# Optimization experiments

Measured on AMD Instinct MI355X. Metric: run time of the kernel, lower is better.

Reference implementation:

```python
import jax, jax.numpy as jnp
import numpy as np

CANVAS_W = 1024.0
CANVAS_H = 1024.0
EPS = 1e-8
GOLDEN = 1.618
ALIGN_THRESH = 5.0


def _mse(p, t):
    return jnp.mean((p - t) ** 2)


def _smooth_l1(p, t):
    d = jnp.abs(p - t)
    return jnp.mean(jnp.where(d < 1.0, 0.5 * d * d, d - 0.5))


def setup_inputs() -> dict:
    key = jax.random.key(0)
    k1, k2, k3, k4 = jax.random.split(key, 4)
    B, N, D = 64, 256, 6
    return {
        "predicted_noise": jax.random.normal(k1, (B, N, D), dtype=jnp.float32),
        "target_noise": jax.random.normal(k2, (B, N, D), dtype=jnp.float32),
        "predicted_layout": jax.random.normal(k3, (B, N, D), dtype=jnp.float32),
        "target_layout": jax.random.normal(k4, (B, N, D), dtype=jnp.float32),
        "element_mask": jnp.ones((B, N), dtype=jnp.float32),
    }


def _iou_loss(pred, target):
    # boxes are (x, y, w, h)
    px1, py1 = pred[..., 0], pred[..., 1]
    px2, py2 = px1 + pred[..., 2], py1 + pred[..., 3]
    tx1, ty1 = target[..., 0], target[..., 1]
    tx2, ty2 = tx1 + target[..., 2], ty1 + target[..., 3]
    inter = jnp.maximum(jnp.minimum(px2, tx2) - jnp.maximum(px1, tx1), 0.0) * \
            jnp.maximum(jnp.minimum(py2, ty2) - jnp.maximum(py1, ty1), 0.0)
    pa = pred[..., 2] * pred[..., 3]
    ta = target[..., 2] * target[..., 3]
    iou = inter / (pa + ta - inter + EPS)
    return jnp.mean(1.0 - iou)


def _loss(predicted_noise, target_noise, predicted_layout, target_layout, element_mask):
    B, N, _ = predicted_noise.shape
    mask3 = element_mask[..., None]  # [B,N,1]
    pn = predicted_noise * mask3
    tn = target_noise * mask3
    pl = predicted_layout * mask3
    tl = target_layout * mask3

    npairs = N * (N - 1) / 2.0
    tri = jnp.triu(jnp.ones((N, N), dtype=pl.dtype), k=1)  # i<j pair mask
    pair_valid = element_mask[:, :, None] * element_mask[:, None, :]  # [B,N,N]

    # ---- noise loss (SmoothL1) ----
    noise_loss = _smooth_l1(pn, tn)

    # ---- position loss: MSE + 0.5*IoU ----
    position_loss = _mse(pl[..., :4], tl[..., :4]) + 0.5 * _iou_loss(pl[..., :4], tl[..., :4])

    # ---- layer loss: MSE + 0.3*pairwise ranking BCE ----
    p_layer, t_layer = pl[..., 4], tl[..., 4]
    diff = p_layer[:, None, :] - p_layer[:, :, None]          # [b,i,j] = p_j - p_i
    y = (t_layer[:, :, None] < t_layer[:, None, :]).astype(pl.dtype)
    # BCE(sigmoid(diff), y): -log sigmoid(d)=softplus(-d); torch clamps log terms at 100
    bce = y * jnp.minimum(jax.nn.softplus(-diff), 100.0) + \
          (1.0 - y) * jnp.minimum(jax.nn.softplus(diff), 100.0)
    ranking = jnp.sum(bce * tri) / (B * npairs)
    layer_loss = _mse(p_layer, t_layer) + 0.3 * ranking

    # ---- confidence loss ----
    confidence_loss = _mse(pl[..., 5], tl[..., 5])

    # ---- aesthetic loss ----
    aspect = pl[..., 2] / (pl[..., 3] + EPS)
    golden = jnp.mean(jnp.abs(aspect - GOLDEN))
    areas = pl[..., 2] * pl[..., 3] * element_mask
    size_harm = jnp.mean(jnp.std(areas, axis=1, ddof=1)) / (jnp.mean(areas) + EPS)
    cx = (pl[..., 0] + pl[..., 2] / 2) * element_mask
    cy = (pl[..., 1] + pl[..., 3] / 2) * element_mask
    valid_count = jnp.sum(element_mask, axis=1, keepdims=True)  # [B,1]
    # NOTE: faithful to original broadcasting ([B] / [B,1] -> [B,B])
    ocx = jnp.sum(cx, axis=1) / (valid_count + EPS)
    ocy = jnp.sum(cy, axis=1) / (valid_count + EPS)
    balance = jnp.mean(jnp.abs(ocx - CANVAS_W / 2) / (CANVAS_W / 2) +
                       jnp.abs(ocy - CANVAS_H / 2) / (CANVAS_H / 2))
    aesthetic_loss = 0.1 * golden + 0.2 * size_harm + 0.15 * balance

    # ---- overlap loss (pairwise) ----
    x1, y1, w, h = pl[..., 0], pl[..., 1], pl[..., 2], pl[..., 3]
    x2, y2 = x1 + w, y1 + h
    iw = jnp.maximum(jnp.minimum(x2[:, :, None], x2[:, None, :]) -
                     jnp.maximum(x1[:, :, None], x1[:, None, :]), 0.0)
    ih = jnp.maximum(jnp.minimum(y2[:, :, None], y2[:, None, :]) -
                     jnp.maximum(y1[:, :, None], y1[:, None, :]), 0.0)
    area = w * h
    min_area = jnp.minimum(area[:, :, None], area[:, None, :])
    overlap_ratio = (iw * ih) / (min_area + EPS) * pair_valid
    overlap_loss = jnp.sum(overlap_ratio * tri) / (B * npairs)

    # ---- alignment loss (6 edge types, pairwise) ----
    edges = jnp.stack([x1, x2, y1, y2, x1 + w / 2, y1 + h / 2], axis=0)  # [6,B,N]
    dist = jnp.abs(edges[:, :, :, None] - edges[:, :, None, :])          # [6,B,N,N]
    pen = jnp.where(dist < ALIGN_THRESH, dist / ALIGN_THRESH, 0.0) * pair_valid[None]
    alignment_loss = jnp.sum(pen * tri) / (B * 6.0 * npairs)

    total = (noise_loss + 1.0 * position_loss + 0.5 * layer_loss +
             0.3 * confidence_loss + 0.2 * aesthetic_loss +
             0.8 * overlap_loss + 0.4 * alignment_loss)
    return total


def reference(predicted_noise, target_noise, predicted_layout, target_layout, element_mask):
    return _loss(predicted_noise, target_noise, predicted_layout, target_layout, element_mask)
```

## Files before the change

kernel.cpp:

```cpp
#include <hip/hip_runtime.h>
#include <math.h>

#define NB 64
#define NN 256
#define NPAIRS 32640.0f
#define EPSF 1e-8f

#define PB(q) ((q) * 64)
#define PW(q) (704 + (q) * 512)

__device__ __forceinline__ float block_sum(float v, float* sred) {
    const int tid = threadIdx.x;
    #pragma unroll
    for (int off = 32; off > 0; off >>= 1) v += __shfl_down(v, off, 64);
    __syncthreads();
    if ((tid & 63) == 0) sred[tid >> 6] = v;
    __syncthreads();
    return sred[0] + sred[1] + sred[2] + sred[3];
}

__device__ __forceinline__ void block_sum3(float a, float b, float c, float* sred,
                                           float& ra, float& rb, float& rc) {
    const int tid = threadIdx.x;
    #pragma unroll
    for (int off = 32; off > 0; off >>= 1) {
        a += __shfl_down(a, off, 64);
        b += __shfl_down(b, off, 64);
        c += __shfl_down(c, off, 64);
    }
    __syncthreads();
    if ((tid & 63) == 0) {
        const int w = tid >> 6;
        sred[w] = a; sred[4 + w] = b; sred[8 + w] = c;
    }
    __syncthreads();
    ra = sred[0] + sred[1] + sred[2]  + sred[3];
    rb = sred[4] + sred[5] + sred[6]  + sred[7];
    rc = sred[8] + sred[9] + sred[10] + sred[11];
}

__global__ __launch_bounds__(256) void loss_main(
    const float* __restrict__ pn, const float* __restrict__ tn,
    const float* __restrict__ pl, const float* __restrict__ tl,
    const float* __restrict__ mask, float* __restrict__ ws)
{
    __shared__ float4 sA[NN], sB[NN];
    __shared__ float2 sC[NN];
    __shared__ float sred[12];

    const int b     = blockIdx.x >> 3;
    const int chunk = blockIdx.x & 7;
    const int i     = threadIdx.x;
    const int e     = b * NN + i;
    const float m   = mask[e];

    const float2* pl2 = (const float2*)pl;
    const float2* tl2 = (const float2*)tl;
    const int r2 = e * 3;
    const float2 pla = pl2[r2 + 0], plb = pl2[r2 + 1], plc = pl2[r2 + 2];
    const float2 tlc = tl2[r2 + 2];

    const float p0 = pla.x * m, p1 = pla.y * m,
                p2 = plb.x * m, p3 = plb.y * m,
                p4 = plc.x * m, p5 = plc.y * m;
    const float t4 = tlc.x * m, t5 = tlc.y * m;

    const float x2v = p0 + p2, y2v = p1 + p3;
    const float areav = p2 * p3;
    const float cxe = p0 + 0.5f * p2, cye = p1 + 0.5f * p3;

    sA[i] = make_float4(p0, p1, x2v, y2v);
    sB[i] = make_float4(cxe, cye, areav, p4);
    sC[i] = make_float2(t4, m);
    __syncthreads();

    float rank = 0.f, ovl = 0.f, aln = 0.f;
    const int dd0 = chunk * 16 + 1;
    #pragma unroll 8
    for (int dd = dd0; dd < dd0 + 16; ++dd) {
        int j = (i + dd) & 255;
        if (dd == 128 && i >= 128) continue;
        float4 aj = sA[j];
        float4 bj = sB[j];
        float2 cj = sC[j];
        float pv = m * cj.y;
        float ow = fmaxf(fminf(x2v, aj.z) - fmaxf(p0, aj.x), 0.f);
        float oh = fmaxf(fminf(y2v, aj.w) - fmaxf(p1, aj.y), 0.f);
        ovl += ow * oh / (fminf(areav, bj.z) + EPSF) * pv;
        float pen = 0.f, d;
        d = fabsf(p0  - aj.x); pen += (d < 5.f) ? d : 0.f;
        d = fabsf(x2v - aj.z); pen += (d < 5.f) ? d : 0.f;
        d = fabsf(p1  - aj.y); pen += (d < 5.f) ? d : 0.f;
        d = fabsf(y2v - aj.w); pen += (d < 5.f) ? d : 0.f;
        d = fabsf(cxe - bj.x); pen += (d < 5.f) ? d : 0.f;
        d = fabsf(cye - bj.y); pen += (d < 5.f) ? d : 0.f;
        aln += pen * 0.2f * pv;
        bool ilt = (i < j);
        float dlo = ilt ? (bj.w - p4) : (p4 - bj.w);
        float ylo = (ilt ? (t4 < cj.x) : (cj.x < t4)) ? 1.f : 0.f;
        float sp  = __logf(1.f + __expf(-fabsf(dlo)));
        float sp_pos = sp + fmaxf(dlo, 0.f);
        float sp_neg = sp + fmaxf(-dlo, 0.f);
        rank += ylo * fminf(sp_neg, 100.f) + (1.f - ylo) * fminf(sp_pos, 100.f);
    }

    {
        float sr, so, sa;
        block_sum3(rank, ovl, aln, sred, sr, so, sa);
        if (i == 0) {
            ws[PW(0) + blockIdx.x] = sr;
            ws[PW(1) + blockIdx.x] = so;
            ws[PW(2) + blockIdx.x] = sa;
        }
    }

    float s;
    switch (chunk) {
    case 0: {
        const float2* pn2 = (const float2*)pn;
        const float2* tn2 = (const float2*)tn;
        float noise = 0.f;
        #pragma unroll
        for (int k = 0; k < 3; ++k) {
            float2 a = pn2[r2 + k], bb = tn2[r2 + k];
            float d0 = fabsf(a.x * m - bb.x * m);
            float d1 = fabsf(a.y * m - bb.y * m);
            noise += (d0 < 1.f) ? 0.5f * d0 * d0 : d0 - 0.5f;
            noise += (d1 < 1.f) ? 0.5f * d1 * d1 : d1 - 0.5f;
        }
        s = block_sum(noise, sred); if (i == 0) ws[PB(0) + b] = s;
        break; }
    case 1: {
        const float2 tla = tl2[r2 + 0], tlb = tl2[r2 + 1];
        const float t0 = tla.x * m, t1 = tla.y * m,
                    t2 = tlb.x * m, t3 = tlb.y * m;
        float posmse = (p0 - t0) * (p0 - t0) + (p1 - t1) * (p1 - t1)
                     + (p2 - t2) * (p2 - t2) + (p3 - t3) * (p3 - t3);
        const float tx2 = t0 + t2, ty2 = t1 + t3;
        float iw = fmaxf(fminf(x2v, tx2) - fmaxf(p0, t0), 0.f);
        float ih = fmaxf(fminf(y2v, ty2) - fmaxf(p1, t1), 0.f);
        float inter = iw * ih;
        float iouL = 1.f - inter / (areav + t2 * t3 - inter + EPSF);
        float s0, s1, s2;
        block_sum3(posmse, iouL, 0.f, sred, s0, s1, s2);
        if (i == 0) { ws[PB(1) + b] = s0; ws[PB(2) + b] = s1; }
        break; }
    case 2: {
        float lmse = (p4 - t4) * (p4 - t4);
        float cmse = (p5 - t5) * (p5 - t5);
        float s0, s1, s2;
        block_sum3(lmse, cmse, 0.f, sred, s0, s1, s2);
        if (i == 0) { ws[PB(3) + b] = s0; ws[PB(4) + b] = s1; }
        break; }
    case 3: {
        float golden = fabsf(p2 / (p3 + EPSF) - 1.618f);
        s = block_sum(golden, sred); if (i == 0) ws[PB(5) + b] = s;
        break; }
    case 4: {
        float areaA = areav * m;
        s = block_sum(areaA, sred); if (i == 0) ws[PB(6) + b] = s;
        break; }
    case 5: {
        float areaA = areav * m;
        s = block_sum(areaA * areaA, sred); if (i == 0) ws[PB(7) + b] = s;
        break; }
    case 6: {
        float cxA = cxe * m, cyA = cye * m;
        float s0, s1, s2;
        block_sum3(cxA, cyA, 0.f, sred, s0, s1, s2);
        if (i == 0) { ws[PB(8) + b] = s0; ws[PB(9) + b] = s1; }
        break; }
    default: {
        s = block_sum(m, sred); if (i == 0) ws[PB(10) + b] = s;
        break; }
    }
}

__global__ __launch_bounds__(256) void loss_final(
    const float* __restrict__ ws, float* __restrict__ out)
{
    __shared__ float sred[12];
    __shared__ float bcx[NB], bcy[NB], bvc[NB];
    const int t = threadIdx.x;

    float v_noise = 0.f, v_pos = 0.f, v_iou = 0.f, v_lm = 0.f, v_cf = 0.f,
          v_go = 0.f, v_ar = 0.f, v_std = 0.f;
    if (t < NB) {
        v_noise = ws[PB(0) + t];
        v_pos   = ws[PB(1) + t];
        v_iou   = ws[PB(2) + t];
        v_lm    = ws[PB(3) + t];
        v_cf    = ws[PB(4) + t];
        v_go    = ws[PB(5) + t];
        v_ar    = ws[PB(6) + t];
        float a2 = ws[PB(7) + t];
        float var = (a2 - v_ar * v_ar * (1.f / 256.f)) * (1.f / 255.f);
        v_std = sqrtf(fmaxf(var, 0.f));
        bcx[t] = ws[PB(8) + t];
        bcy[t] = ws[PB(9) + t];
        bvc[t] = ws[PB(10) + t];
    }
    float v_rank = ws[PW(0) + t] + ws[PW(0) + 256 + t];
    float v_ovl  = ws[PW(1) + t] + ws[PW(1) + 256 + t];
    float v_aln  = ws[PW(2) + t] + ws[PW(2) + 256 + t];
    __syncthreads();

    float v_bal = 0.f;
    if (t < NB) {
        float inv = 1.f / (bvc[t] + EPSF);
        for (int j = 0; j < NB; ++j) {
            v_bal += fabsf(bcx[j] * inv - 512.f) * (1.f / 512.f)
                   + fabsf(bcy[j] * inv - 512.f) * (1.f / 512.f);
        }
    }

    float S_noise, S_pos, S_iou, S_lm, S_cf, S_go, S_ar, S_std, S_bal,
          S_rank, S_ovl, S_aln;
    block_sum3(v_noise, v_pos, v_iou, sred, S_noise, S_pos, S_iou);
    block_sum3(v_lm,    v_cf,  v_go,  sred, S_lm,    S_cf,  S_go);
    block_sum3(v_ar,    v_std, v_bal, sred, S_ar,    S_std, S_bal);
    block_sum3(v_rank,  v_ovl, v_aln, sred, S_rank,  S_ovl, S_aln);

    if (t == 0) {
        const float BN = 64.f * 256.f;
        float noise_loss = S_noise / (BN * 6.f);
        float position   = S_pos / (BN * 4.f) + 0.5f * (S_iou / BN);
        float layer      = S_lm / BN + 0.3f * (S_rank / (64.f * NPAIRS));
        float conf       = S_cf / BN;
        float golden     = S_go / BN;
        float size_harm  = (S_std / 64.f) / (S_ar / BN + EPSF);
        float balance    = S_bal / 4096.f;
        float aes        = 0.1f * golden + 0.2f * size_harm + 0.15f * balance;
        float ovl        = S_ovl / (64.f * NPAIRS);
        float aln        = S_aln / (64.f * 6.f * NPAIRS);
        out[0] = noise_loss + position + 0.5f * layer + 0.3f * conf
               + 0.2f * aes + 0.8f * ovl + 0.4f * aln;
    }
}

extern "C" void kernel_launch(void* const* d_in, const int* in_sizes, int n_in,
                              void* d_out, int out_size, void* d_ws, size_t ws_size,
                              hipStream_t stream) {
    const float* pn   = (const float*)d_in[0];
    const float* tn   = (const float*)d_in[1];
    const float* pl   = (const float*)d_in[2];
    const float* tl   = (const float*)d_in[3];
    const float* mask = (const float*)d_in[4];
    float* ws  = (float*)d_ws;
    float* out = (float*)d_out;
    hipLaunchKernelGGL(loss_main, dim3(512), dim3(256), 0, stream,
                       pn, tn, pl, tl, mask, ws);
    hipLaunchKernelGGL(loss_final, dim3(1), dim3(256), 0, stream, ws, out);
}
```

Measured before the change: 71.79 us.

## Split pairwise work into 16 chunks per batch and simplify final reduction

Doubles the grid to 1024 blocks so each block handles 8 pair offsets instead of 16, and spreads the per-element side terms across 11 chunks with one block reduction each. The final kernel shrinks to a single 64-thread wavefront that uses shuffles instead of shared memory and block barriers. This targets latency from too few blocks relative to the CU count and from serial reductions. In exchange, every block reloads and stages the whole batch into shared memory, so redundant loads double, and the final kernel now sums 16 partials per slot.

After: 71.37 us. Within noise of the previous version (-0.6%).

```diff
diff --git a/kernel.cpp b/kernel.cpp
--- a/kernel.cpp
+++ b/kernel.cpp
@@ -7,7 +7,7 @@
 #define EPSF 1e-8f
 
 #define PB(q) ((q) * 64)
-#define PW(q) (704 + (q) * 512)
+#define PW(q) (704 + (q) * 1024)
 
 __device__ __forceinline__ float block_sum(float v, float* sred) {
     const int tid = threadIdx.x;
@@ -37,6 +37,12 @@
     ra = sred[0] + sred[1] + sred[2]  + sred[3];
     rb = sred[4] + sred[5] + sred[6]  + sred[7];
     rc = sred[8] + sred[9] + sred[10] + sred[11];
+}
+
+__device__ __forceinline__ float wave_sum(float v) {
+    #pragma unroll
+    for (int off = 32; off > 0; off >>= 1) v += __shfl_down(v, off, 64);
+    return v;
 }
 
 __global__ __launch_bounds__(256) void loss_main(
@@ -48,8 +54,8 @@
     __shared__ float2 sC[NN];
     __shared__ float sred[12];
 
-    const int b     = blockIdx.x >> 3;
-    const int chunk = blockIdx.x & 7;
+    const int b     = blockIdx.x >> 4;
+    const int chunk = blockIdx.x & 15;
     const int i     = threadIdx.x;
     const int e     = b * NN + i;
     const float m   = mask[e];
@@ -75,9 +81,10 @@
     __syncthreads();
 
     float rank = 0.f, ovl = 0.f, aln = 0.f;
-    const int dd0 = chunk * 16 + 1;
-    #pragma unroll 8
-    for (int dd = dd0; dd < dd0 + 16; ++dd) {
+    const int dd0 = chunk * 8 + 1;
+    #pragma unroll
+    for (int k = 0; k < 8; ++k) {
+        const int dd = dd0 + k;
         int j = (i + dd) & 255;
         if (dd == 128 && i >= 128) continue;
         float4 aj = sA[j];
@@ -114,7 +121,8 @@
         }
     }
 
-    float s;
+    float v = 0.f;
+    bool have = true;
     switch (chunk) {
     case 0: {
         const float2* pn2 = (const float2*)pn;
@@ -128,98 +136,89 @@
             noise += (d0 < 1.f) ? 0.5f * d0 * d0 : d0 - 0.5f;
             noise += (d1 < 1.f) ? 0.5f * d1 * d1 : d1 - 0.5f;
         }
-        s = block_sum(noise, sred); if (i == 0) ws[PB(0) + b] = s;
+        v = noise;
         break; }
     case 1: {
         const float2 tla = tl2[r2 + 0], tlb = tl2[r2 + 1];
         const float t0 = tla.x * m, t1 = tla.y * m,
                     t2 = tlb.x * m, t3 = tlb.y * m;
-        float posmse = (p0 - t0) * (p0 - t0) + (p1 - t1) * (p1 - t1)
-                     + (p2 - t2) * (p2 - t2) + (p3 - t3) * (p3 - t3);
+        v = (p0 - t0) * (p0 - t0) + (p1 - t1) * (p1 - t1)
+          + (p2 - t2) * (p2 - t2) + (p3 - t3) * (p3 - t3);
+        break; }
+    case 2: {
+        const float2 tla = tl2[r2 + 0], tlb = tl2[r2 + 1];
+        const float t0 = tla.x * m, t1 = tla.y * m,
+                    t2 = tlb.x * m, t3 = tlb.y * m;
         const float tx2 = t0 + t2, ty2 = t1 + t3;
         float iw = fmaxf(fminf(x2v, tx2) - fmaxf(p0, t0), 0.f);
         float ih = fmaxf(fminf(y2v, ty2) - fmaxf(p1, t1), 0.f);
         float inter = iw * ih;
-        float iouL = 1.f - inter / (areav + t2 * t3 - inter + EPSF);
-        float s0, s1, s2;
-        block_sum3(posmse, iouL, 0.f, sred, s0, s1, s2);
-        if (i == 0) { ws[PB(1) + b] = s0; ws[PB(2) + b] = s1; }
+        v = 1.f - inter / (areav + t2 * t3 - inter + EPSF);
         break; }
-    case 2: {
-        float lmse = (p4 - t4) * (p4 - t4);
-        float cmse = (p5 - t5) * (p5 - t5);
-        float s0, s1, s2;
-        block_sum3(lmse, cmse, 0.f, sred, s0, s1, s2);
-        if (i == 0) { ws[PB(3) + b] = s0; ws[PB(4) + b] = s1; }
-        break; }
-    case 3: {
-        float golden = fabsf(p2 / (p3 + EPSF) - 1.618f);
-        s = block_sum(golden, sred); if (i == 0) ws[PB(5) + b] = s;
-        break; }
-    case 4: {
-        float areaA = areav * m;
-        s = block_sum(areaA, sred); if (i == 0) ws[PB(6) + b] = s;
-        break; }
-    case 5: {
-        float areaA = areav * m;
-        s = block_sum(areaA * areaA, sred); if (i == 0) ws[PB(7) + b] = s;
-        break; }
-    case 6: {
-        float cxA = cxe * m, cyA = cye * m;
-        float s0, s1, s2;
-        block_sum3(cxA, cyA, 0.f, sred, s0, s1, s2);
-        if (i == 0) { ws[PB(8) + b] = s0; ws[PB(9) + b] = s1; }
-        break; }
-    default: {
-        s = block_sum(m, sred); if (i == 0) ws[PB(10) + b] = s;
-        break; }
-    }
-}
-
-__global__ __launch_bounds__(256) void loss_final(
+    case 3: v = (p4 - t4) * (p4 - t4); break;
+    case 4: v = (p5 - t5) * (p5 - t5); break;
+    case 5: v = fabsf(p2 / (p3 + EPSF) - 1.618f); break;
+    case 6: v = areav * m; break;
+    case 7: { float a = areav * m; v = a * a; break; }
+    case 8: v = cxe * m; break;
+    case 9: v = cye * m; break;
+    case 10: v = m; break;
+    default: have = false; break;
+    }
+    if (have) {
+        float s = block_sum(v, sred);
+        if (i == 0) ws[PB(chunk) + b] = s;
+    }
+}
+
+__global__ __launch_bounds__(64) void loss_final(
     const float* __restrict__ ws, float* __restrict__ out)
 {
-    __shared__ float sred[12];
-    __shared__ float bcx[NB], bcy[NB], bvc[NB];
     const int t = threadIdx.x;
 
-    float v_noise = 0.f, v_pos = 0.f, v_iou = 0.f, v_lm = 0.f, v_cf = 0.f,
-          v_go = 0.f, v_ar = 0.f, v_std = 0.f;
-    if (t < NB) {
-        v_noise = ws[PB(0) + t];
-        v_pos   = ws[PB(1) + t];
-        v_iou   = ws[PB(2) + t];
-        v_lm    = ws[PB(3) + t];
-        v_cf    = ws[PB(4) + t];
-        v_go    = ws[PB(5) + t];
-        v_ar    = ws[PB(6) + t];
-        float a2 = ws[PB(7) + t];
-        float var = (a2 - v_ar * v_ar * (1.f / 256.f)) * (1.f / 255.f);
-        v_std = sqrtf(fmaxf(var, 0.f));
-        bcx[t] = ws[PB(8) + t];
-        bcy[t] = ws[PB(9) + t];
-        bvc[t] = ws[PB(10) + t];
-    }
-    float v_rank = ws[PW(0) + t] + ws[PW(0) + 256 + t];
-    float v_ovl  = ws[PW(1) + t] + ws[PW(1) + 256 + t];
-    float v_aln  = ws[PW(2) + t] + ws[PW(2) + 256 + t];
-    __syncthreads();
-
+    float v_noise = ws[PB(0) + t];
+    float v_pos   = ws[PB(1) + t];
+    float v_iou   = ws[PB(2) + t];
+    float v_lm    = ws[PB(3) + t];
+    float v_cf    = ws[PB(4) + t];
+    float v_go    = ws[PB(5) + t];
+    float v_ar    = ws[PB(6) + t];
+    float a2      = ws[PB(7) + t];
+    float v_cx    = ws[PB(8) + t];
+    float v_cy    = ws[PB(9) + t];
+    float v_vc    = ws[PB(10) + t];
+    float var   = (a2 - v_ar * v_ar * (1.f / 256.f)) * (1.f / 255.f);
+    float v_std = sqrtf(fmaxf(var, 0.f));
+
+    float v_rank = 0.f, v_ovl = 0.f, v_aln = 0.f;
+    #pragma unroll
+    for (int k = 0; k < 16; ++k) {
+        v_rank += ws[PW(0) + k * 64 + t];
+        v_ovl  += ws[PW(1) + k * 64 + t];
+        v_aln  += ws[PW(2) + k * 64 + t];
+    }
+
+    float inv = 1.f / (v_vc + EPSF);
     float v_bal = 0.f;
-    if (t < NB) {
-        float inv = 1.f / (bvc[t] + EPSF);
-        for (int j = 0; j < NB; ++j) {
-            v_bal += fabsf(bcx[j] * inv - 512.f) * (1.f / 512.f)
-                   + fabsf(bcy[j] * inv - 512.f) * (1.f / 512.f);
-        }
-    }
-
-    float S_noise, S_pos, S_iou, S_lm, S_cf, S_go, S_ar, S_std, S_bal,
-          S_rank, S_ovl, S_aln;
-    block_sum3(v_noise, v_pos, v_iou, sred, S_noise, S_pos, S_iou);
-    block_sum3(v_lm,    v_cf,  v_go,  sred, S_lm,    S_cf,  S_go);
-    block_sum3(v_ar,    v_std, v_bal, sred, S_ar,    S_std, S_bal);
-    block_sum3(v_rank,  v_ovl, v_aln, sred, S_rank,  S_ovl, S_aln);
+    for (int j = 0; j < NB; ++j) {
+        float cxj = __shfl(v_cx, j, 64);
+        float cyj = __shfl(v_cy, j, 64);
+        v_bal += fabsf(cxj * inv - 512.f) * (1.f / 512.f)
+               + fabsf(cyj * inv - 512.f) * (1.f / 512.f);
+    }
+
+    float S_noise = wave_sum(v_noise);
+    float S_pos   = wave_sum(v_pos);
+    float S_iou   = wave_sum(v_iou);
+    float S_lm    = wave_sum(v_lm);
+    float S_cf    = wave_sum(v_cf);
+    float S_go    = wave_sum(v_go);
+    float S_ar    = wave_sum(v_ar);
+    float S_std   = wave_sum(v_std);
+    float S_bal   = wave_sum(v_bal);
+    float S_rank  = wave_sum(v_rank);
+    float S_ovl   = wave_sum(v_ovl);
+    float S_aln   = wave_sum(v_aln);
 
     if (t == 0) {
         const float BN = 64.f * 256.f;
@@ -248,7 +247,7 @@
     const float* mask = (const float*)d_in[4];
     float* ws  = (float*)d_ws;
     float* out = (float*)d_out;
-    hipLaunchKernelGGL(loss_main, dim3(512), dim3(256), 0, stream,
+    hipLaunchKernelGGL(loss_main, dim3(1024), dim3(256), 0, stream,
                        pn, tn, pl, tl, mask, ws);
-    hipLaunchKernelGGL(loss_final, dim3(1), dim3(256), 0, stream, ws, out);
-}
+    hipLaunchKernelGGL(loss_final, dim3(1), dim3(64), 0, stream, ws, out);
+}
```
